# Kernel tuning notes

Hardware: AMD Instinct MI355X
Metric: run time of the kernel (lower is better)

Reference implementation:

```python
import jax, jax.numpy as jnp
import numpy as np

N_NODES = 100000
N_EDGES = 1600000
D = 64


def setup_inputs() -> dict:
    key = jax.random.key(0)
    k1, k2, k3, k4 = jax.random.split(key, 4)
    graph_embedding = jax.random.normal(k1, (N_NODES, D), dtype=jnp.float32)
    # xavier_uniform_ on a (1, D) tensor: bound = sqrt(6 / (1 + D))
    bound = float(np.sqrt(6.0 / (1 + D)))
    weight = jax.random.uniform(k2, (1, D), dtype=jnp.float32, minval=-bound, maxval=bound)
    src = jax.random.randint(k3, (N_EDGES,), 0, N_NODES, dtype=jnp.int32)
    dst = jax.random.randint(k4, (N_EDGES,), 0, N_NODES, dtype=jnp.int32)
    return {"graph_embedding": graph_embedding, "weight": weight, "src": src, "dst": dst}


def reference(graph_embedding, weight, src, dst):
    # emb = elu(x * w) per node, then copy_u/sum over edges:
    # out[d] = sum over edges (s -> d) of emb[s]
    emb = jax.nn.elu(graph_embedding * weight)          # [N, D]
    msgs = emb[src]                                     # [E, D] gathered source messages
    out = jax.ops.segment_sum(msgs, dst, num_segments=graph_embedding.shape[0])
    return out
```

## Files before the change

kernel.cpp:

```cpp
#include <hip/hip_runtime.h>

#define D 64
#define D4 (D / 4)
#define SBSHIFT 8
#define SBROWS 256
#define CHUNK_E 4096
#define STAGE_CAP 4608
#define NCH_MAX 512
#define NSB_MAX 512

typedef float f32x4 __attribute__((ext_vector_type(4)));

__device__ __forceinline__ float elu1(float z) {
    return z > 0.0f ? z : expm1f(z);
}

__device__ __forceinline__ unsigned int bfpair(float a, float b) {
    unsigned int ua = __float_as_uint(a);
    unsigned int ub = __float_as_uint(b);
    ua = (ua + 0x7FFFu + ((ua >> 16) & 1u)) >> 16;
    ub = (ub + 0x7FFFu + ((ub >> 16) & 1u)) & 0xFFFF0000u;
    return ub | ua;
}

__device__ __forceinline__ float bl16(int u) {
    return __uint_as_float((unsigned)u << 16);
}
__device__ __forceinline__ float bh16(int u) {
    return __uint_as_float((unsigned)u & 0xFFFF0000u);
}

__global__ __launch_bounds__(512) void chunk_emb_kernel(
        const float* __restrict__ x, const float* __restrict__ w,
        uint4* __restrict__ emb16,
        const int* __restrict__ src, const int* __restrict__ dst,
        int* __restrict__ slots_lin,
        int* __restrict__ cbase,
        int total8, int n_edges, int NSB) {
    __shared__ int hist[NSB_MAX], base[NSB_MAX], cur[NSB_MAX];
    __shared__ int wsum[8];
    __shared__ int stage[CHUNK_E];
    const int tid = threadIdx.x;
    const int lane = tid & 63, wid = tid >> 6;

    hist[tid] = 0;
    const int gsz = gridDim.x * 512;
    for (int i = blockIdx.x * 512 + tid; i < total8; i += gsz) {
        f32x4 a = __builtin_nontemporal_load((const f32x4*)x + 2 * i);
        f32x4 b = __builtin_nontemporal_load((const f32x4*)x + 2 * i + 1);
        float4 wa = ((const float4*)w)[(2 * i) & 15];
        float4 wb = ((const float4*)w)[(2 * i + 1) & 15];
        uint4 o;
        o.x = bfpair(elu1(a.x * wa.x), elu1(a.y * wa.y));
        o.y = bfpair(elu1(a.z * wa.z), elu1(a.w * wa.w));
        o.z = bfpair(elu1(b.x * wb.x), elu1(b.y * wb.y));
        o.w = bfpair(elu1(b.z * wb.z), elu1(b.w * wb.w));
        emb16[i] = o;
    }

    const int c0  = blockIdx.x * CHUNK_E;
    const int kn  = min(CHUNK_E, n_edges - c0);
    const int kn4 = kn >> 2;
    const int tail = kn & 3;
    __syncthreads();
    const int4* dst4 = (const int4*)(dst + c0);
    for (int k = tid; k < kn4; k += 512) {
        int4 dv = dst4[k];
        atomicAdd(&hist[dv.x >> SBSHIFT], 1);
        atomicAdd(&hist[dv.y >> SBSHIFT], 1);
        atomicAdd(&hist[dv.z >> SBSHIFT], 1);
        atomicAdd(&hist[dv.w >> SBSHIFT], 1);
    }
    if (tid < tail)
        atomicAdd(&hist[dst[c0 + (kn4 << 2) + tid] >> SBSHIFT], 1);
    __syncthreads();
    int h = hist[tid];
    int incl = h;
    #pragma unroll
    for (int off = 1; off < 64; off <<= 1) {
        int t = __shfl_up(incl, off, 64);
        if (lane >= off) incl += t;
    }
    if (lane == 63) wsum[wid] = incl;
    __syncthreads();
    {
        int pre = 0;
        for (int k = 0; k < wid; k++) pre += wsum[k];
        int e = pre + incl - h;
        base[tid] = e;
        cur[tid]  = e;
    }
    __syncthreads();
    const int4* src4 = (const int4*)(src + c0);
    for (int k = tid; k < kn4; k += 512) {
        int4 dv = dst4[k];
        int4 sv = src4[k];
        int pos;
        pos = atomicAdd(&cur[dv.x >> SBSHIFT], 1);
        stage[pos] = ((dv.x & (SBROWS - 1)) << 17) | sv.x;
        pos = atomicAdd(&cur[dv.y >> SBSHIFT], 1);
        stage[pos] = ((dv.y & (SBROWS - 1)) << 17) | sv.y;
        pos = atomicAdd(&cur[dv.z >> SBSHIFT], 1);
        stage[pos] = ((dv.z & (SBROWS - 1)) << 17) | sv.z;
        pos = atomicAdd(&cur[dv.w >> SBSHIFT], 1);
        stage[pos] = ((dv.w & (SBROWS - 1)) << 17) | sv.w;
    }
    if (tid < tail) {
        int k = (kn4 << 2) + tid;
        int d = dst[c0 + k], s = src[c0 + k];
        int pos = atomicAdd(&cur[d >> SBSHIFT], 1);
        stage[pos] = ((d & (SBROWS - 1)) << 17) | s;
    }
    __syncthreads();
    for (int j = tid; j < kn; j += 512)
        slots_lin[c0 + j] = stage[j];
    if (tid < NSB) cbase[blockIdx.x * (NSB + 1) + tid] = base[tid];
    if (tid == 0)  cbase[blockIdx.x * (NSB + 1) + NSB] = kn;
}

__global__ __launch_bounds__(512) void fine_sort_kernel(
        const int* __restrict__ slots_lin,
        const int* __restrict__ cbase,
        int* __restrict__ sorted2,
        int* __restrict__ node_off,
        int n_nodes, int NCH, int NSB) {
    __shared__ int rstart[NCH_MAX], rc[NCH_MAX];
    __shared__ int counts[SBROWS], cur[SBROWS];
    __shared__ int wsum[4], swa[8], swt[8];
    __shared__ int stage_out[STAGE_CAP];
    const int s = blockIdx.x;
    const int tid = threadIdx.x;
    const int wid = tid >> 6, lane = tid & 63;
    const int sg = tid >> 4, l16 = tid & 15;

    int va = 0, vt = 0;
    if (tid < NCH) {
        int a = cbase[tid * (NSB + 1) + s];
        int b = cbase[tid * (NSB + 1) + s + 1];
        rstart[tid] = tid * CHUNK_E + a;
        rc[tid] = b - a;
        va = a;
        vt = b - a;
    }
    #pragma unroll
    for (int off = 1; off < 64; off <<= 1) {
        va += __shfl_xor(va, off, 64);
        vt += __shfl_xor(vt, off, 64);
    }
    if (lane == 0) { swa[wid] = va; swt[wid] = vt; }
    if (tid < SBROWS) counts[tid] = 0;
    __syncthreads();
    int sbb = 0, T = 0;
    #pragma unroll
    for (int k = 0; k < 8; k++) { sbb += swa[k]; T += swt[k]; }
    const bool fast = (T <= STAGE_CAP);
    for (int c = sg; c < NCH; c += 32) {
        int n = rc[c], st = rstart[c];
        for (int j = l16; j < n; j += 16)
            atomicAdd(&counts[((unsigned)slots_lin[st + j]) >> 17], 1);
    }
    __syncthreads();
    int v = 0, incl = 0;
    if (tid < SBROWS) {
        v = counts[tid];
        incl = v;
        #pragma unroll
        for (int off = 1; off < 64; off <<= 1) {
            int t = __shfl_up(incl, off, 64);
            if (lane >= off) incl += t;
        }
        if (lane == 63) wsum[wid] = incl;
    }
    __syncthreads();
    if (tid < SBROWS) {
        int pre = 0;
        for (int k = 0; k < wid; k++) pre += wsum[k];
        int e0 = pre + incl - v;
        cur[tid] = fast ? e0 : sbb + e0;
        int g0 = (s << SBSHIFT) + tid;
        if (g0 < n_nodes) node_off[g0] = sbb + e0;
    }
    if (s == gridDim.x - 1 && tid == 0) node_off[n_nodes] = sbb + T;
    __syncthreads();
    for (int c = sg; c < NCH; c += 32) {
        int n = rc[c], st = rstart[c];
        for (int j = l16; j < n; j += 16) {
            int pl = slots_lin[st + j];
            int r = ((unsigned)pl) >> 17;
            int pos = atomicAdd(&cur[r], 1);
            if (fast) stage_out[pos] = pl & 0x1FFFF;
            else      sorted2[pos]   = pl & 0x1FFFF;
        }
    }
    __syncthreads();
    if (fast) {
        for (int i = tid; i < T; i += 512)
            sorted2[sbb + i] = stage_out[i];
    }
}

__device__ __forceinline__ int pick_idx(int p, int m0, int m1, int m2,
                                        const int* __restrict__ s2, int W0) {
    int a  = __shfl(m0, p & 63, 64);
    int b  = __shfl(m1, p & 63, 64);
    int cc = __shfl(m2, p & 63, 64);
    int r = p < 64 ? a : (p < 128 ? b : cc);
    if (p >= 192) r = s2[W0 + p];
    return r;
}

__global__ void gather_sum_kernel(const unsigned int* __restrict__ emb16,
                                  const int* __restrict__ sorted2,
                                  const int* __restrict__ node_off,
                                  float* __restrict__ out, int n_nodes) {
    const int wv = (blockIdx.x * blockDim.x + threadIdx.x) >> 6;
    const int lane = threadIdx.x & 63;
    const int g = lane >> 3;
    const int c = lane & 7;
    const int n0 = wv * 8;
    if (n0 >= n_nodes) return;
    const int n = n0 + g;

    int beg = 0, end = 0;
    if (n < n_nodes) {
        beg = node_off[n];
        end = node_off[n + 1];
    }
    const int W0   = node_off[n0];
    const int Wend = node_off[min(n0 + 8, n_nodes)];
    const int T = Wend - W0;

    int m0 = 0, m1 = 0, m2 = 0;
    if (lane < T)       m0 = sorted2[W0 + lane];
    if (64 + lane < T)  m1 = sorted2[W0 + 64 + lane];
    if (128 + lane < T) m2 = sorted2[W0 + 128 + lane];

    const int4* row = (const int4*)emb16;
    const int pb = beg - W0;
    const int d = end - beg;
    int dmax = d;
    dmax = max(dmax, __shfl_xor(dmax, 8, 64));
    dmax = max(dmax, __shfl_xor(dmax, 16, 64));
    dmax = max(dmax, __shfl_xor(dmax, 32, 64));
    const int pclamp = T - 1;

    float acc[8] = {0.f, 0.f, 0.f, 0.f, 0.f, 0.f, 0.f, 0.f};

    int e = 0;
    for (; e + 4 <= dmax; e += 4) {
        int p0 = min(max(pb + e,     0), pclamp);
        int p1 = min(max(pb + e + 1, 0), pclamp);
        int p2 = min(max(pb + e + 2, 0), pclamp);
        int p3 = min(max(pb + e + 3, 0), pclamp);
        int i0 = pick_idx(p0, m0, m1, m2, sorted2, W0);
        int i1 = pick_idx(p1, m0, m1, m2, sorted2, W0);
        int i2 = pick_idx(p2, m0, m1, m2, sorted2, W0);
        int i3 = pick_idx(p3, m0, m1, m2, sorted2, W0);
        int4 u0 = make_int4(0, 0, 0, 0);
        int4 u1 = make_int4(0, 0, 0, 0);
        int4 u2 = make_int4(0, 0, 0, 0);
        int4 u3 = make_int4(0, 0, 0, 0);
        if (e < d)     u0 = row[i0 * 8 + c];
        if (e + 1 < d) u1 = row[i1 * 8 + c];
        if (e + 2 < d) u2 = row[i2 * 8 + c];
        if (e + 3 < d) u3 = row[i3 * 8 + c];
        acc[0] += bl16(u0.x) + bl16(u1.x) + bl16(u2.x) + bl16(u3.x);
        acc[1] += bh16(u0.x) + bh16(u1.x) + bh16(u2.x) + bh16(u3.x);
        acc[2] += bl16(u0.y) + bl16(u1.y) + bl16(u2.y) + bl16(u3.y);
        acc[3] += bh16(u0.y) + bh16(u1.y) + bh16(u2.y) + bh16(u3.y);
        acc[4] += bl16(u0.z) + bl16(u1.z) + bl16(u2.z) + bl16(u3.z);
        acc[5] += bh16(u0.z) + bh16(u1.z) + bh16(u2.z) + bh16(u3.z);
        acc[6] += bl16(u0.w) + bl16(u1.w) + bl16(u2.w) + bl16(u3.w);
        acc[7] += bh16(u0.w) + bh16(u1.w) + bh16(u2.w) + bh16(u3.w);
    }
    for (; e < dmax; ++e) {
        int p0 = min(max(pb + e, 0), pclamp);
        int i0 = pick_idx(p0, m0, m1, m2, sorted2, W0);
        if (e < d) {
            int4 u0 = row[i0 * 8 + c];
            acc[0] += bl16(u0.x); acc[1] += bh16(u0.x);
            acc[2] += bl16(u0.y); acc[3] += bh16(u0.y);
            acc[4] += bl16(u0.z); acc[5] += bh16(u0.z);
            acc[6] += bl16(u0.w); acc[7] += bh16(u0.w);
        }
    }

    if (n < n_nodes) {
        f32x4* out4 = (f32x4*)out;
        f32x4 o0 = {acc[0], acc[1], acc[2], acc[3]};
        f32x4 o1 = {acc[4], acc[5], acc[6], acc[7]};
        __builtin_nontemporal_store(o0, out4 + (size_t)n * D4 + c * 2);
        __builtin_nontemporal_store(o1, out4 + (size_t)n * D4 + c * 2 + 1);
    }
}

__global__ void zero_out_kernel(float* __restrict__ out, int total4) {
    int i = blockIdx.x * blockDim.x + threadIdx.x;
    if (i < total4) ((float4*)out)[i] = make_float4(0.f, 0.f, 0.f, 0.f);
}

__global__ void scatter_fused_kernel(const float* __restrict__ x,
                                     const float* __restrict__ w,
                                     const int* __restrict__ src,
                                     const int* __restrict__ dst,
                                     float* __restrict__ out, int n_edges) {
    int t = blockIdx.x * blockDim.x + threadIdx.x;
    int e = t >> 4;
    int c = t & 15;
    if (e >= n_edges) return;
    int s = src[e];
    int d = dst[e];
    float4 xv = ((const float4*)x)[s * D4 + c];
    float4 wv = ((const float4*)w)[c];
    float* o = out + d * D + c * 4;
    unsafeAtomicAdd(o + 0, elu1(xv.x * wv.x));
    unsafeAtomicAdd(o + 1, elu1(xv.y * wv.y));
    unsafeAtomicAdd(o + 2, elu1(xv.z * wv.z));
    unsafeAtomicAdd(o + 3, elu1(xv.w * wv.w));
}

extern "C" void kernel_launch(void* const* d_in, const int* in_sizes, int n_in,
                              void* d_out, int out_size, void* d_ws, size_t ws_size,
                              hipStream_t stream) {
    const float* x   = (const float*)d_in[0];
    const float* w   = (const float*)d_in[1];
    const int*   src = (const int*)d_in[2];
    const int*   dst = (const int*)d_in[3];
    float* out = (float*)d_out;

    const int n_nodes = in_sizes[0] / D;
    const int n_edges = in_sizes[2];
    const int total4  = n_nodes * D4;
    const int total8  = n_nodes * 8;
    const int block = 256;

    const int NSB = (n_nodes + SBROWS - 1) >> SBSHIFT;
    const int NCH = (n_edges + CHUNK_E - 1) / CHUNK_E;

    auto align16 = [](size_t v) { return (v + 15) & ~size_t(15); };
    const size_t emb_b      = align16((size_t)n_nodes * D * 2);
    const size_t slots_b    = align16((size_t)NCH * CHUNK_E * 4);
    const size_t cbase_b    = align16((size_t)NCH * (NSB + 1) * 4);
    const size_t sorted2_b  = align16((size_t)n_edges * 4);
    const size_t nodeoff_b  = align16((size_t)(n_nodes + 1) * 4);
    const size_t need = emb_b + slots_b + cbase_b + sorted2_b + nodeoff_b;

    if (ws_size >= need && n_nodes <= 131072 && NSB <= NSB_MAX && NCH <= NCH_MAX) {
        char* p = (char*)d_ws;
        unsigned int* emb16 = (unsigned int*)p;  p += emb_b;
        int* slots_lin = (int*)p;  p += slots_b;
        int* cbase     = (int*)p;  p += cbase_b;
        int* sorted2   = (int*)p;  p += sorted2_b;
        int* node_off  = (int*)p;

        chunk_emb_kernel<<<NCH, 512, 0, stream>>>(
            x, w, (uint4*)emb16, src, dst, slots_lin, cbase,
            total8, n_edges, NSB);
        fine_sort_kernel<<<NSB, 512, 0, stream>>>(
            slots_lin, cbase, sorted2, node_off, n_nodes, NCH, NSB);
        const int nwaves = (n_nodes + 7) / 8;
        const int gblocks = (nwaves * 64 + block - 1) / block;
        gather_sum_kernel<<<gblocks, block, 0, stream>>>(
            emb16, sorted2, node_off, out, n_nodes);
    } else {
        zero_out_kernel<<<(total4 + block - 1) / block, block, 0, stream>>>(out, total4);
        const int nt = n_edges * 16;
        scatter_fused_kernel<<<(nt + block - 1) / block, block, 0, stream>>>(
            x, w, src, dst, out, n_edges);
    }
}
```

Measured before the change: 141.0 us.

## Split bf16 embeddings into two column planes and dedicate blocks to embedding

The bf16 embedding table is now stored as two planes, each holding 32 of the 64 columns, and the gather kernel launches twice as many blocks, each handling one plane with 8-byte loads per lane. Each plane is half the size of the old table, which is meant to make the random row gathers hit cache more often and to expose more parallelism. The embedding computation also moves from being interleaved in every chunk block to a separate set of extra blocks in the same launch, so the histogram blocks no longer wait on it. In exchange, node offsets and index lists are read twice, and each gathered row segment is half as wide.

```diff
diff --git a/kernel.cpp b/kernel.cpp
--- a/kernel.cpp
+++ b/kernel.cpp
@@ -8,6 +8,7 @@
 #define STAGE_CAP 4608
 #define NCH_MAX 512
 #define NSB_MAX 512
+#define EMB_BLOCKS 192
 
 typedef float f32x4 __attribute__((ext_vector_type(4)));
 
@@ -32,33 +33,40 @@
 
 __global__ __launch_bounds__(512) void chunk_emb_kernel(
         const float* __restrict__ x, const float* __restrict__ w,
-        uint4* __restrict__ emb16,
+        unsigned int* __restrict__ emb16,
         const int* __restrict__ src, const int* __restrict__ dst,
         int* __restrict__ slots_lin,
         int* __restrict__ cbase,
-        int total8, int n_edges, int NSB) {
+        int total8, int n_edges, int NSB, int NCH, int n_nodes) {
     __shared__ int hist[NSB_MAX], base[NSB_MAX], cur[NSB_MAX];
     __shared__ int wsum[8];
     __shared__ int stage[CHUNK_E];
     const int tid = threadIdx.x;
     const int lane = tid & 63, wid = tid >> 6;
+    const int bid = blockIdx.x;
+
+    if (bid >= NCH) {
+        uint4* p0 = (uint4*)emb16;
+        uint4* p1 = (uint4*)(emb16 + (size_t)n_nodes * 16);
+        for (int i = (bid - NCH) * 512 + tid; i < total8; i += EMB_BLOCKS * 512) {
+            const int n = i >> 3, c = i & 7;
+            f32x4 a = __builtin_nontemporal_load((const f32x4*)x + 2 * i);
+            f32x4 b = __builtin_nontemporal_load((const f32x4*)x + 2 * i + 1);
+            float4 wa = ((const float4*)w)[(2 * i) & 15];
+            float4 wb = ((const float4*)w)[(2 * i + 1) & 15];
+            uint4 o;
+            o.x = bfpair(elu1(a.x * wa.x), elu1(a.y * wa.y));
+            o.y = bfpair(elu1(a.z * wa.z), elu1(a.w * wa.w));
+            o.z = bfpair(elu1(b.x * wb.x), elu1(b.y * wb.y));
+            o.w = bfpair(elu1(b.z * wb.z), elu1(b.w * wb.w));
+            uint4* pl = (c < 4) ? p0 : p1;
+            pl[n * 4 + (c & 3)] = o;
+        }
+        return;
+    }
 
     hist[tid] = 0;
-    const int gsz = gridDim.x * 512;
-    for (int i = blockIdx.x * 512 + tid; i < total8; i += gsz) {
-        f32x4 a = __builtin_nontemporal_load((const f32x4*)x + 2 * i);
-        f32x4 b = __builtin_nontemporal_load((const f32x4*)x + 2 * i + 1);
-        float4 wa = ((const float4*)w)[(2 * i) & 15];
-        float4 wb = ((const float4*)w)[(2 * i + 1) & 15];
-        uint4 o;
-        o.x = bfpair(elu1(a.x * wa.x), elu1(a.y * wa.y));
-        o.y = bfpair(elu1(a.z * wa.z), elu1(a.w * wa.w));
-        o.z = bfpair(elu1(b.x * wb.x), elu1(b.y * wb.y));
-        o.w = bfpair(elu1(b.z * wb.z), elu1(b.w * wb.w));
-        emb16[i] = o;
-    }
-
-    const int c0  = blockIdx.x * CHUNK_E;
+    const int c0  = bid * CHUNK_E;
     const int kn  = min(CHUNK_E, n_edges - c0);
     const int kn4 = kn >> 2;
     const int tail = kn & 3;
@@ -114,8 +122,8 @@
     __syncthreads();
     for (int j = tid; j < kn; j += 512)
         slots_lin[c0 + j] = stage[j];
-    if (tid < NSB) cbase[blockIdx.x * (NSB + 1) + tid] = base[tid];
-    if (tid == 0)  cbase[blockIdx.x * (NSB + 1) + NSB] = kn;
+    if (tid < NSB) cbase[bid * (NSB + 1) + tid] = base[tid];
+    if (tid == 0)  cbase[bid * (NSB + 1) + NSB] = kn;
 }
 
 __global__ __launch_bounds__(512) void fine_sort_kernel(
@@ -186,8 +194,8 @@
         int n = rc[c], st = rstart[c];
         for (int j = l16; j < n; j += 16) {
             int pl = slots_lin[st + j];
-            int r = ((unsigned)pl) >> 17;
-            int pos = atomicAdd(&cur[r], 1);
+            int r2 = ((unsigned)pl) >> 17;
+            int pos = atomicAdd(&cur[r2], 1);
             if (fast) stage_out[pos] = pl & 0x1FFFF;
             else      sorted2[pos]   = pl & 0x1FFFF;
         }
@@ -212,8 +220,11 @@
 __global__ void gather_sum_kernel(const unsigned int* __restrict__ emb16,
                                   const int* __restrict__ sorted2,
                                   const int* __restrict__ node_off,
-                                  float* __restrict__ out, int n_nodes) {
-    const int wv = (blockIdx.x * blockDim.x + threadIdx.x) >> 6;
+                                  float* __restrict__ out, int n_nodes,
+                                  int pbk) {
+    const int plane = (blockIdx.x >= pbk) ? 1 : 0;
+    const int lb = blockIdx.x - plane * pbk;
+    const int wv = (lb * (int)blockDim.x + (int)threadIdx.x) >> 6;
     const int lane = threadIdx.x & 63;
     const int g = lane >> 3;
     const int c = lane & 7;
@@ -235,7 +246,7 @@
     if (64 + lane < T)  m1 = sorted2[W0 + 64 + lane];
     if (128 + lane < T) m2 = sorted2[W0 + 128 + lane];
 
-    const int4* row = (const int4*)emb16;
+    const int2* rowh = (const int2*)(emb16 + (size_t)plane * (size_t)n_nodes * 16);
     const int pb = beg - W0;
     const int d = end - beg;
     int dmax = d;
@@ -244,7 +255,7 @@
     dmax = max(dmax, __shfl_xor(dmax, 32, 64));
     const int pclamp = T - 1;
 
-    float acc[8] = {0.f, 0.f, 0.f, 0.f, 0.f, 0.f, 0.f, 0.f};
+    float a0 = 0.f, a1 = 0.f, a2 = 0.f, a3 = 0.f;
 
     int e = 0;
     for (; e + 4 <= dmax; e += 4) {
@@ -256,41 +267,33 @@
         int i1 = pick_idx(p1, m0, m1, m2, sorted2, W0);
         int i2 = pick_idx(p2, m0, m1, m2, sorted2, W0);
         int i3 = pick_idx(p3, m0, m1, m2, sorted2, W0);
-        int4 u0 = make_int4(0, 0, 0, 0);
-        int4 u1 = make_int4(0, 0, 0, 0);
-        int4 u2 = make_int4(0, 0, 0, 0);
-        int4 u3 = make_int4(0, 0, 0, 0);
-        if (e < d)     u0 = row[i0 * 8 + c];
-        if (e + 1 < d) u1 = row[i1 * 8 + c];
-        if (e + 2 < d) u2 = row[i2 * 8 + c];
-        if (e + 3 < d) u3 = row[i3 * 8 + c];
-        acc[0] += bl16(u0.x) + bl16(u1.x) + bl16(u2.x) + bl16(u3.x);
-        acc[1] += bh16(u0.x) + bh16(u1.x) + bh16(u2.x) + bh16(u3.x);
-        acc[2] += bl16(u0.y) + bl16(u1.y) + bl16(u2.y) + bl16(u3.y);
-        acc[3] += bh16(u0.y) + bh16(u1.y) + bh16(u2.y) + bh16(u3.y);
-        acc[4] += bl16(u0.z) + bl16(u1.z) + bl16(u2.z) + bl16(u3.z);
-        acc[5] += bh16(u0.z) + bh16(u1.z) + bh16(u2.z) + bh16(u3.z);
-        acc[6] += bl16(u0.w) + bl16(u1.w) + bl16(u2.w) + bl16(u3.w);
-        acc[7] += bh16(u0.w) + bh16(u1.w) + bh16(u2.w) + bh16(u3.w);
+        int2 u0 = make_int2(0, 0);
+        int2 u1 = make_int2(0, 0);
+        int2 u2 = make_int2(0, 0);
+        int2 u3 = make_int2(0, 0);
+        if (e < d)     u0 = rowh[i0 * 8 + c];
+        if (e + 1 < d) u1 = rowh[i1 * 8 + c];
+        if (e + 2 < d) u2 = rowh[i2 * 8 + c];
+        if (e + 3 < d) u3 = rowh[i3 * 8 + c];
+        a0 += bl16(u0.x) + bl16(u1.x) + bl16(u2.x) + bl16(u3.x);
+        a1 += bh16(u0.x) + bh16(u1.x) + bh16(u2.x) + bh16(u3.x);
+        a2 += bl16(u0.y) + bl16(u1.y) + bl16(u2.y) + bl16(u3.y);
+        a3 += bh16(u0.y) + bh16(u1.y) + bh16(u2.y) + bh16(u3.y);
     }
     for (; e < dmax; ++e) {
         int p0 = min(max(pb + e, 0), pclamp);
         int i0 = pick_idx(p0, m0, m1, m2, sorted2, W0);
         if (e < d) {
-            int4 u0 = row[i0 * 8 + c];
-            acc[0] += bl16(u0.x); acc[1] += bh16(u0.x);
-            acc[2] += bl16(u0.y); acc[3] += bh16(u0.y);
-            acc[4] += bl16(u0.z); acc[5] += bh16(u0.z);
-            acc[6] += bl16(u0.w); acc[7] += bh16(u0.w);
+            int2 u0 = rowh[i0 * 8 + c];
+            a0 += bl16(u0.x); a1 += bh16(u0.x);
+            a2 += bl16(u0.y); a3 += bh16(u0.y);
         }
     }
 
     if (n < n_nodes) {
         f32x4* out4 = (f32x4*)out;
-        f32x4 o0 = {acc[0], acc[1], acc[2], acc[3]};
-        f32x4 o1 = {acc[4], acc[5], acc[6], acc[7]};
-        __builtin_nontemporal_store(o0, out4 + (size_t)n * D4 + c * 2);
-        __builtin_nontemporal_store(o1, out4 + (size_t)n * D4 + c * 2 + 1);
+        f32x4 o = {a0, a1, a2, a3};
+        __builtin_nontemporal_store(o, out4 + (size_t)n * D4 + plane * 8 + c);
     }
 }
 
@@ -353,15 +356,15 @@
         int* sorted2   = (int*)p;  p += sorted2_b;
         int* node_off  = (int*)p;
 
-        chunk_emb_kernel<<<NCH, 512, 0, stream>>>(
-            x, w, (uint4*)emb16, src, dst, slots_lin, cbase,
-            total8, n_edges, NSB);
+        chunk_emb_kernel<<<NCH + EMB_BLOCKS, 512, 0, stream>>>(
+            x, w, emb16, src, dst, slots_lin, cbase,
+            total8, n_edges, NSB, NCH, n_nodes);
         fine_sort_kernel<<<NSB, 512, 0, stream>>>(
             slots_lin, cbase, sorted2, node_off, n_nodes, NCH, NSB);
         const int nwaves = (n_nodes + 7) / 8;
-        const int gblocks = (nwaves * 64 + block - 1) / block;
-        gather_sum_kernel<<<gblocks, block, 0, stream>>>(
-            emb16, sorted2, node_off, out, n_nodes);
+        const int pbk = (nwaves * 64 + block - 1) / block;
+        gather_sum_kernel<<<2 * pbk, block, 0, stream>>>(
+            emb16, sorted2, node_off, out, n_nodes, pbk);
     } else {
         zero_out_kernel<<<(total4 + block - 1) / block, block, 0, stream>>>(out, total4);
         const int nt = n_edges * 16;
```

New measurement: 153.2 us. 1.09x slower.
